# Kernel tuning notes

Hardware: AMD Instinct MI355X
Metric: run time of the kernel (lower is better)

## Reference

```python
import jax, jax.numpy as jnp
import numpy as np

K = 27        # num_neighs
EPS = 1e-5    # BatchNorm eps (torch default)
LATENT = 256


def _knn_idx(pts, k):
    # pts: (B, N, 3) -> (B, N, k) indices of k nearest points (self included, dist 0),
    # matching torch_cluster.knn(x, x, k).
    d = jnp.sum((pts[:, :, None, :] - pts[:, None, :, :]) ** 2, axis=-1)  # (B, N, N)
    _, idx = jax.lax.top_k(-d, k)
    return idx


def _graph_feature(x, idx):
    # x: (B, C, N), idx: (B, N, K) -> (B, 2C, N, K) = concat(neigh - center, center)
    xt = jnp.transpose(x, (0, 2, 1))               # (B, N, C)
    neigh = jax.vmap(lambda p, i: p[i])(xt, idx)   # (B, N, K, C) gather
    center = xt[:, :, None, :]                     # (B, N, 1, C)
    feat = jnp.concatenate([neigh - center, jnp.broadcast_to(center, neigh.shape)], axis=-1)
    return jnp.transpose(feat, (0, 3, 1, 2))       # (B, 2C, N, K)


def _bn_lrelu(x, gamma, beta, axes):
    # Training-mode BatchNorm (biased batch stats over `axes`, channel = dim 1) + LeakyReLU(0.2)
    mean = jnp.mean(x, axis=axes, keepdims=True)
    var = jnp.var(x, axis=axes, keepdims=True)
    shape = [1] * x.ndim
    shape[1] = -1
    y = (x - mean) * jax.lax.rsqrt(var + EPS) * gamma.reshape(shape) + beta.reshape(shape)
    return jnp.where(y >= 0, y, 0.2 * y)


def setup_inputs() -> dict:
    key = jax.random.key(0)
    ks = jax.random.split(key, 6)
    B, T, N = 2, 2, 256
    x = jax.random.normal(ks[0], (B, T, N, 3), dtype=jnp.float32)
    # Conv2d(1x1) channel ladder for depth=4, bb_size=24, input_features=6
    dims = [(6, 48), (192, 192), (768, 768), (3072, 3072)]
    inp = {"x": x}
    for i, (cin, cout) in enumerate(dims):
        inp[f"w{i}"] = jax.random.normal(ks[i + 1], (cout, cin), dtype=jnp.float32) * 0.05
        inp[f"g{i}"] = jnp.ones((cout,), jnp.float32)
        inp[f"b{i}"] = jnp.zeros((cout,), jnp.float32)
    # final Conv1d(8160 -> latent): 8160 = 48*(2+8+32+128)
    inp["w4"] = jax.random.normal(ks[5], (LATENT, 8160), dtype=jnp.float32) * 0.02
    inp["g4"] = jnp.ones((LATENT,), jnp.float32)
    inp["b4"] = jnp.zeros((LATENT,), jnp.float32)
    return inp


def reference(x, w0, g0, b0, w1, g1, b1, w2, g2, b2, w3, g3, b3, w4, g4, b4):
    B, T, N, _ = x.shape
    flat = x.reshape(B * T, N, 3)
    idx = _knn_idx(flat, K)  # fixed neighbors reused at every depth (only_true_neighs=True)
    cur = _graph_feature(jnp.transpose(flat, (0, 2, 1)), idx)  # (BT, 6, N, K)
    outs = []
    for w, g, b in [(w0, g0, b0), (w1, g1, b1), (w2, g2, b2), (w3, g3, b3)]:
        if outs:
            cur = _graph_feature(outs[-1], idx)      # (BT, 2C_prev, N, K)
        h = jnp.einsum('bcnk,oc->bonk', cur, w)      # 1x1 conv, no bias
        h = _bn_lrelu(h, g, b, axes=(0, 2, 3))
        hmax = jnp.max(h, axis=-1)                   # max over K neighbors -> (BT, C, N)
        C = hmax.shape[1]
        exp = hmax.reshape(B, T, C, N)
        # Faithful to source: avgpool does `out, _ = x.mean(dim=1, keepdim=True)` which
        # tuple-unpacks the batch dim (requires B==2): out = batch-0 temporal mean (1, C, N),
        # then expanded to (B, T, C, N).
        tp = jnp.mean(exp, axis=1, keepdims=True)[0]  # (1, C, N)
        comb = jnp.concatenate([exp, jnp.broadcast_to(tp[None], exp.shape)], axis=2)  # (B,T,2C,N)
        outs.append(comb.reshape(B * T, 2 * C, N))
    xcat = jnp.concatenate(outs, axis=1)             # (BT, 8160, N)
    y = jnp.einsum('bcn,oc->bon', xcat, w4)          # 1x1 conv1d
    y = _bn_lrelu(y, g4, b4, axes=(0, 2))
    return y.reshape(B, T, LATENT, N)
```

## Files before the change

kernel.cpp:

```cpp
#include <hip/hip_runtime.h>
#include <hip/hip_bf16.h>

#define NPTS 256
#define NB   4
#define KNN  27
#define EPSV 1e-5f

typedef unsigned short u16;
typedef _Float16 f16;
typedef __attribute__((ext_vector_type(8))) _Float16 f16x8;
typedef __attribute__((ext_vector_type(4))) _Float16 f16x4;
typedef __attribute__((ext_vector_type(4))) float f32x4;

#define OFF_IDX    0
#define OFF_XYZ    131072
#define OFF_A0     262144
#define OFF_A1     270336
#define OFF_A2     344064
#define OFF_A3     1523712
#define OFF_A4     20398080
#define OFF_PQ     24576000
#define OFF_SLICE  74907648
#define OFF_XC     100073472
#define OFF_Y      116785152

typedef __attribute__((address_space(3))) unsigned int lds_u32_t;
typedef __attribute__((address_space(1))) unsigned int glb_u32_t;

__device__ __forceinline__ void gload16(const f16* g, const u16* l) {
    __builtin_amdgcn_global_load_lds((const glb_u32_t*)g, (lds_u32_t*)(u16*)l, 16, 0, 0);
}

__device__ __forceinline__ float dist3_nocontract(float ax, float ay, float az,
                                                  float bx, float by, float bz) {
#pragma clang fp contract(off)
    float dx = bx - ax, dy = by - ay, dz = bz - az;
    float s = dx * dx;
    s = s + dy * dy;
    s = s + dz * dz;
    return s;
}

__global__ __launch_bounds__(256) void knn_prep(
    const float* __restrict__ x, int* __restrict__ idx, f16* __restrict__ xyz,
    const float* __restrict__ w0, const float* __restrict__ w1,
    const float* __restrict__ w2, const float* __restrict__ w3,
    const float* __restrict__ w4, char* __restrict__ ws)
{
    int bid = blockIdx.x;
    int tid = threadIdx.x;

    if (bid < 4096 && (bid & 3) == 3) {
        if (tid >= 64) return;
        int pt = bid >> 2;
        int b = pt >> 8, n = pt & 255;
        int lane = tid;

        float xp0 = x[pt * 3 + 0];
        float xp1 = x[pt * 3 + 1];
        float xp2 = x[pt * 3 + 2];

        if (lane < 32) {
            float v = (lane < 3) ? x[pt * 3 + lane] : 0.f;
            xyz[((long)b * NPTS + n) * 32 + lane] = (f16)v;
        }

        unsigned long long key[4];
#pragma unroll
        for (int u = 0; u < 4; ++u) {
            int j = lane + 64 * u;
            int gj = b * NPTS + j;
            float d = dist3_nocontract(xp0, xp1, xp2,
                                       x[gj * 3 + 0], x[gj * 3 + 1], x[gj * 3 + 2]);
            key[u] = ((unsigned long long)__float_as_uint(d) << 32) | (unsigned int)j;
        }

        for (int r = 0; r < KNN; ++r) {
            unsigned long long m = key[0];
            m = key[1] < m ? key[1] : m;
            m = key[2] < m ? key[2] : m;
            m = key[3] < m ? key[3] : m;
#pragma unroll
            for (int off = 32; off; off >>= 1) {
                unsigned long long o = __shfl_xor(m, off);
                m = o < m ? o : m;
            }
            if (lane == 0) idx[pt * 28 + r] = (int)(m & 0xffffffffu);
#pragma unroll
            for (int u = 0; u < 4; ++u)
                if (key[u] == m) key[u] = ~0ULL;
        }
        return;
    }

    int pbid = (bid < 4096) ? (bid - (bid >> 2)) : (bid - 1024);

    if (pbid == 0) {
        f16* A = (f16*)(ws + OFF_A0);
        int jj = tid >> 2;
        int cc = (tid & 3) * 8;
        if (jj < 48) {
            f16x8 lo = {}, df = {};
#pragma unroll
            for (int j = 0; j < 8; ++j) {
                int c = cc + j;
                if (c < 3) {
                    float a = w0[jj * 6 + c];
                    float b2 = w0[jj * 6 + 3 + c];
                    lo[j] = (f16)a;
                    df[j] = (f16)(b2 - a);
                }
            }
            *(f16x8*)&A[jj * 32 + cc] = lo;
            *(f16x8*)&A[(48 + jj) * 32 + cc] = df;
        }
        if (jj < 32) {
            f16x8 z = {};
            *(f16x8*)&A[(96 + jj) * 32 + cc] = z;
        }
        return;
    }
    if (pbid < 13) {
        f16* A = (f16*)(ws + OFF_A1);
        int j = (pbid - 1) * 16 + (tid >> 4);
        int cc = (tid & 15) * 8;
        if (cc >= 96) return;
        f32x4 a0 = *(const f32x4*)&w1[j * 192 + cc];
        f32x4 a1 = *(const f32x4*)&w1[j * 192 + cc + 4];
        f32x4 b0 = *(const f32x4*)&w1[j * 192 + 96 + cc];
        f32x4 b1 = *(const f32x4*)&w1[j * 192 + 96 + cc + 4];
        f16x8 lo, df;
#pragma unroll
        for (int j2 = 0; j2 < 4; ++j2) {
            lo[j2] = (f16)a0[j2];     lo[4 + j2] = (f16)a1[j2];
            df[j2] = (f16)(b0[j2] - a0[j2]);
            df[4 + j2] = (f16)(b1[j2] - a1[j2]);
        }
        *(f16x8*)&A[j * 96 + cc] = lo;
        *(f16x8*)&A[(192 + j) * 96 + cc] = df;
        return;
    }
    if (pbid < 205) {
        f16* A = (f16*)(ws + OFF_A2);
        int j = (pbid - 13) * 4 + (tid >> 6);
        int cc = (tid & 63) * 8;
        if (cc >= 384) return;
        f32x4 a0 = *(const f32x4*)&w2[(long)j * 768 + cc];
        f32x4 a1 = *(const f32x4*)&w2[(long)j * 768 + cc + 4];
        f32x4 b0 = *(const f32x4*)&w2[(long)j * 768 + 384 + cc];
        f32x4 b1 = *(const f32x4*)&w2[(long)j * 768 + 384 + cc + 4];
        f16x8 lo, df;
#pragma unroll
        for (int j2 = 0; j2 < 4; ++j2) {
            lo[j2] = (f16)a0[j2];     lo[4 + j2] = (f16)a1[j2];
            df[j2] = (f16)(b0[j2] - a0[j2]);
            df[4 + j2] = (f16)(b1[j2] - a1[j2]);
        }
        *(f16x8*)&A[(long)j * 384 + cc] = lo;
        *(f16x8*)&A[(long)(768 + j) * 384 + cc] = df;
        return;
    }
    if (pbid < 3277) {
        f16* A = (f16*)(ws + OFF_A3);
        int j = pbid - 205;
        int cc = tid * 8;
        if (cc >= 1536) return;
        f32x4 a0 = *(const f32x4*)&w3[(long)j * 3072 + cc];
        f32x4 a1 = *(const f32x4*)&w3[(long)j * 3072 + cc + 4];
        f32x4 b0 = *(const f32x4*)&w3[(long)j * 3072 + 1536 + cc];
        f32x4 b1 = *(const f32x4*)&w3[(long)j * 3072 + 1536 + cc + 4];
        f16x8 lo, df;
#pragma unroll
        for (int j2 = 0; j2 < 4; ++j2) {
            lo[j2] = (f16)a0[j2];     lo[4 + j2] = (f16)a1[j2];
            df[j2] = (f16)(b0[j2] - a0[j2]);
            df[4 + j2] = (f16)(b1[j2] - a1[j2]);
        }
        *(f16x8*)&A[(long)j * 1536 + cc] = lo;
        *(f16x8*)&A[(long)(3072 + j) * 1536 + cc] = df;
        return;
    }
    {
        f16* A = (f16*)(ws + OFF_A4);
        int loc = pbid - 3277;
        int r = loc >> 2;
        int c0 = (loc & 3) * 2048 + tid * 8;
        if (c0 >= 8160) return;
        f32x4 a0 = *(const f32x4*)&w4[(long)r * 8160 + c0];
        f32x4 a1 = *(const f32x4*)&w4[(long)r * 8160 + c0 + 4];
        f16x8 hv;
#pragma unroll
        for (int j2 = 0; j2 < 4; ++j2) {
            hv[j2] = (f16)a0[j2];
            hv[4 + j2] = (f16)a1[j2];
        }
        *(f16x8*)&A[(long)r * 8160 + c0] = hv;
        return;
    }
}

__global__ __launch_bounds__(256) void gemm_mfma(
    const f16* __restrict__ A, const f16* __restrict__ B,
    float* __restrict__ out, int M, int Kpad, int K,
    int ldF, long bsF, long bsO, int nsplit, long pstride)
{
    __shared__ u16 sA[2][128 * 32];
    __shared__ u16 sB[2][128 * 32];

    int bz = blockIdx.z;
    int b = bz / nsplit, slice = bz - b * nsplit;
    int kchunk = (((K + nsplit - 1) / nsplit) + 31) & ~31;
    int kstart = slice * kchunk;
    int kend = K < kstart + kchunk ? K : kstart + kchunk;
    int nt = (kend - kstart) >> 5;

    const f16* pB = B + (long)b * bsF;
    float* Ob = out + (long)slice * pstride + (long)b * bsO;

    int m0 = blockIdx.x * 128, n0 = blockIdx.y * 128;
    int tid = threadIdx.x, lane = tid & 63, wid = tid >> 6;
    int wm = (wid >> 1) * 64, wn = (wid & 1) * 64;
    int lrow = lane & 15, quad = lane >> 4;

    int r0 = wid * 16 + (lane >> 2);
    int r1 = 64 + r0;
    int ck = lane & 3;
    int c0 = (ck ^ ((r0 >> 1) & 3)) * 8;
    int c1 = (ck ^ ((r1 >> 1) & 3)) * 8;

    const f16* gA0 = A + (long)(m0 + r0) * Kpad + c0 + kstart;
    const f16* gA1 = A + (long)(m0 + r1) * Kpad + c1 + kstart;
    const f16* gB0 = pB + (long)(n0 + r0) * ldF + c0 + kstart;
    const f16* gB1 = pB + (long)(n0 + r1) * ldF + c1 + kstart;

    int oA0 = (wid * 16) * 32;
    int oA1 = (64 + wid * 16) * 32;

    int fs = (quad ^ ((lrow >> 1) & 3)) * 8;
    int offA = (wm + lrow) * 32 + fs;
    int offB = (wn + lrow) * 32 + fs;

    f32x4 acc[4][4] = {};

    gload16(gA0, &sA[0][oA0]);
    gload16(gA1, &sA[0][oA1]);
    gload16(gB0, &sB[0][oA0]);
    gload16(gB1, &sB[0][oA1]);
    gA0 += 32; gA1 += 32; gB0 += 32; gB1 += 32;
    asm volatile("s_waitcnt vmcnt(0)" ::: "memory");
    __builtin_amdgcn_s_barrier();

    for (int t = 0; t < nt - 1; ++t) {
        int cur = t & 1, nxt = cur ^ 1;
        gload16(gA0, &sA[nxt][oA0]);
        gload16(gA1, &sA[nxt][oA1]);
        gload16(gB0, &sB[nxt][oA0]);
        gload16(gB1, &sB[nxt][oA1]);
        gA0 += 32; gA1 += 32; gB0 += 32; gB1 += 32;

        f16x8 fb[4];
#pragma unroll
        for (int nt4 = 0; nt4 < 4; ++nt4)
            fb[nt4] = *(const f16x8*)&sB[cur][offB + nt4 * 512];
        __builtin_amdgcn_s_setprio(1);
#pragma unroll
        for (int mt = 0; mt < 4; ++mt) {
            f16x8 fa = *(const f16x8*)&sA[cur][offA + mt * 512];
#pragma unroll
            for (int nt4 = 0; nt4 < 4; ++nt4)
                acc[mt][nt4] = __builtin_amdgcn_mfma_f32_16x16x32_f16(fa, fb[nt4], acc[mt][nt4], 0, 0, 0);
        }
        __builtin_amdgcn_s_setprio(0);

        asm volatile("s_waitcnt vmcnt(0) lgkmcnt(0)" ::: "memory");
        __builtin_amdgcn_s_barrier();
    }

    {
        int cur = (nt - 1) & 1;
        f16x8 fb[4];
#pragma unroll
        for (int nt4 = 0; nt4 < 4; ++nt4)
            fb[nt4] = *(const f16x8*)&sB[cur][offB + nt4 * 512];
#pragma unroll
        for (int mt = 0; mt < 4; ++mt) {
            f16x8 fa = *(const f16x8*)&sA[cur][offA + mt * 512];
#pragma unroll
            for (int nt4 = 0; nt4 < 4; ++nt4)
                acc[mt][nt4] = __builtin_amdgcn_mfma_f32_16x16x32_f16(fa, fb[nt4], acc[mt][nt4], 0, 0, 0);
        }
    }

#pragma unroll
    for (int mt = 0; mt < 4; ++mt)
#pragma unroll
        for (int nt4 = 0; nt4 < 4; ++nt4) {
            int C = n0 + wn + nt4 * 16 + lrow;
            int Rb = m0 + wm + mt * 16 + quad * 4;
#pragma unroll
            for (int r = 0; r < 4; ++r) {
                int R = Rb + r;
                if (R < M) Ob[(long)R * NPTS + C] = acc[mt][nt4][r];
            }
        }
}

__global__ __launch_bounds__(512) void gather_finalize(
    const float* __restrict__ PQ, long pstride, int nsplit,
    const int* __restrict__ idx,
    const float* __restrict__ g, const float* __restrict__ beta,
    f16* __restrict__ slice, int Co)
{
    __shared__ float p_sh[NB][NPTS];
    __shared__ float val_sh[NB][NPTS];
    __shared__ float red[2][NB][2];
    int o = blockIdx.x;
    int tid = threadIdx.x;
    int b = tid >> 7;
    int l128 = tid & 127;
    int wh = (tid >> 6) & 1;

    long ip0 = ((long)b * 2 * Co + o) * NPTS;
    long iq0 = ((long)b * 2 * Co + Co + o) * NPTS;

    float qv[2];
#pragma unroll
    for (int u = 0; u < 2; ++u) {
        int n = l128 + 128 * u;
        float v = 0.f, q = 0.f;
        for (int sp2 = 0; sp2 < nsplit; ++sp2) {
            v += PQ[sp2 * pstride + ip0 + n];
            q += PQ[sp2 * pstride + iq0 + n];
        }
        p_sh[b][n] = v;
        qv[u] = q;
    }
    __syncthreads();

    float mx[2], mn[2];
    float s = 0.f, ss = 0.f;
#pragma unroll
    for (int u = 0; u < 2; ++u) {
        int n = l128 + 128 * u;
        const int4* ip4 = (const int4*)(idx + ((long)b * NPTS + n) * 28);
        int nb[28];
#pragma unroll
        for (int w = 0; w < 7; ++w) {
            int4 t = ip4[w];
            nb[4 * w] = t.x; nb[4 * w + 1] = t.y;
            nb[4 * w + 2] = t.z; nb[4 * w + 3] = t.w;
        }
        float sp = 0.f, spp = 0.f;
        float pmx = -__builtin_inff(), pmn = __builtin_inff();
#pragma unroll
        for (int k = 0; k < KNN; ++k) {
            float p = p_sh[b][nb[k]];
            sp += p;
            spp = fmaf(p, p, spp);
            pmx = fmaxf(pmx, p);
            pmn = fminf(pmn, p);
        }
        float q = qv[u];
        s += sp + 27.f * q;
        ss += spp + q * fmaf(2.f, sp, 27.f * q);
        mx[u] = pmx + q;
        mn[u] = pmn + q;
    }
#pragma unroll
    for (int off = 32; off; off >>= 1) {
        s += __shfl_xor(s, off);
        ss += __shfl_xor(ss, off);
    }
    if ((tid & 63) == 0) { red[0][b][wh] = s; red[1][b][wh] = ss; }
    __syncthreads();

    float ts = ((red[0][0][0] + red[0][0][1]) + (red[0][1][0] + red[0][1][1]))
             + ((red[0][2][0] + red[0][2][1]) + (red[0][3][0] + red[0][3][1]));
    float tss = ((red[1][0][0] + red[1][0][1]) + (red[1][1][0] + red[1][1][1]))
              + ((red[1][2][0] + red[1][2][1]) + (red[1][3][0] + red[1][3][1]));
    const float cnt = (float)(NB * NPTS * KNN);
    float mean = ts / cnt;
    float var = tss / cnt - mean * mean;
    float sc = g[o] * (1.0f / sqrtf(var + EPSV));
    float tt = beta[o] - mean * sc;

#pragma unroll
    for (int u = 0; u < 2; ++u) {
        int n = l128 + 128 * u;
        float v = (sc >= 0.f) ? mx[u] : mn[u];
        float z = sc * v + tt;
        val_sh[b][n] = z >= 0.f ? z : 0.2f * z;
    }
    __syncthreads();

    long ro = ((long)b * 2 * Co + o) * NPTS;
    long rt = ((long)b * 2 * Co + Co + o) * NPTS;
#pragma unroll
    for (int u = 0; u < 2; ++u) {
        int n = l128 + 128 * u;
        float tp = 0.5f * (val_sh[0][n] + val_sh[1][n]);
        slice[ro + n] = (f16)val_sh[b][n];
        slice[rt + n] = (f16)tp;
    }
}

__global__ __launch_bounds__(256) void transpose_cn(
    const f16* __restrict__ slice, f16* __restrict__ xc,
    int Ctot, int offc)
{
    __shared__ u16 t[32][36];
    int c0 = blockIdx.x * 32, n0 = blockIdx.y * 32, b = blockIdx.z;
    const f16* S = slice + (long)b * Ctot * NPTS;
    int tid = threadIdx.x;
    int r = tid >> 3, s4 = (tid & 7) * 4;

    f16x4 v = *(const f16x4*)&S[(long)(c0 + r) * NPTS + n0 + s4];
    t[r][s4 + 0] = ((const u16*)&v)[0];
    t[r][s4 + 1] = ((const u16*)&v)[1];
    t[r][s4 + 2] = ((const u16*)&v)[2];
    t[r][s4 + 3] = ((const u16*)&v)[3];
    __syncthreads();

    long base = ((long)b * NPTS + n0 + r) * 8160 + offc + c0 + s4;
    f16x4 hv;
    u16* hp = (u16*)&hv;
#pragma unroll
    for (int j = 0; j < 4; ++j) hp[j] = t[s4 + j][r];
    *(f16x4*)&xc[base] = hv;
}

__global__ __launch_bounds__(256) void final_bn(const float* __restrict__ y,
                                                const float* __restrict__ g4,
                                                const float* __restrict__ b4,
                                                float* __restrict__ out) {
    __shared__ float red[8];
    int o = blockIdx.x;
    int tid = threadIdx.x;
    int lane = tid & 63, w = tid >> 6;

    float v[4];
    float s = 0.f, ss = 0.f;
#pragma unroll
    for (int b = 0; b < 4; ++b) {
        float acc = 0.f;
#pragma unroll
        for (int sp = 0; sp < 16; ++sp)
            acc += y[sp * 262144 + b * 65536 + o * 256 + tid];
        v[b] = acc;
        s += acc;
        ss += acc * acc;
    }
#pragma unroll
    for (int off = 32; off; off >>= 1) {
        s += __shfl_xor(s, off);
        ss += __shfl_xor(ss, off);
    }
    if (lane == 0) { red[w] = s; red[4 + w] = ss; }
    __syncthreads();
    s = (red[0] + red[1]) + (red[2] + red[3]);
    ss = (red[4] + red[5]) + (red[6] + red[7]);
    float mean = s / 1024.f;
    float var = ss / 1024.f - mean * mean;
    float sc = g4[o] * (1.0f / sqrtf(var + EPSV));
    float tt = b4[o] - mean * sc;
#pragma unroll
    for (int b = 0; b < 4; ++b) {
        float z = sc * v[b] + tt;
        z = z >= 0.f ? z : 0.2f * z;
        out[(long)b * 65536 + o * 256 + tid] = z;
    }
}

extern "C" void kernel_launch(void* const* d_in, const int* in_sizes, int n_in,
                              void* d_out, int out_size, void* d_ws, size_t ws_size,
                              hipStream_t stream) {
    const float* x = (const float*)d_in[0];
    const float* wl[4];
    const float* gl[4];
    const float* bl[4];
    for (int i = 0; i < 4; ++i) {
        wl[i] = (const float*)d_in[1 + 3 * i];
        gl[i] = (const float*)d_in[2 + 3 * i];
        bl[i] = (const float*)d_in[3 + 3 * i];
    }
    const float* w4 = (const float*)d_in[13];
    const float* g4 = (const float*)d_in[14];
    const float* b4 = (const float*)d_in[15];

    char* ws = (char*)d_ws;
    int* idx = (int*)(ws + OFF_IDX);
    f16* xyz = (f16*)(ws + OFF_XYZ);
    float* PQ = (float*)(ws + OFF_PQ);
    f16* slice = (f16*)(ws + OFF_SLICE);
    f16* xc = (f16*)(ws + OFF_XC);
    float* y = (float*)(ws + OFF_Y);

    knn_prep<<<dim3(5325), dim3(256), 0, stream>>>(x, idx, xyz,
                                                   wl[0], wl[1], wl[2], wl[3], w4, ws);

    const int Kp[4] = {32, 96, 384, 1536};
    const int Co[4] = {48, 192, 768, 3072};
    const int offc[4] = {0, 96, 480, 2016};
    const int inoff[4] = {0, 0, 96, 480};
    const int nsp[4] = {1, 3, 2, 1};
    const long aoff[4] = {OFF_A0, OFF_A1, OFF_A2, OFF_A3};

    for (int i = 0; i < 4; ++i) {
        int M = 2 * Co[i];
        int Mpad = (M + 127) & ~127;
        const f16* A = (const f16*)(ws + aoff[i]);

        const f16* Bp;
        int ldF;
        long bsF;
        if (i == 0) { Bp = xyz; ldF = 32; bsF = (long)NPTS * 32; }
        else { Bp = xc + inoff[i]; ldF = 8160; bsF = (long)NPTS * 8160; }

        long pstride = (long)NB * M * NPTS;
        gemm_mfma<<<dim3(Mpad / 128, NPTS / 128, NB * nsp[i]), dim3(256), 0, stream>>>(
            A, Bp, PQ, M, Kp[i], Kp[i], ldF, bsF, (long)M * NPTS, nsp[i], pstride);

        gather_finalize<<<dim3(Co[i]), dim3(512), 0, stream>>>(
            PQ, pstride, nsp[i], idx, gl[i], bl[i], slice, Co[i]);
        transpose_cn<<<dim3(M / 32, NPTS / 32, NB), dim3(256), 0, stream>>>(
            slice, xc, M, offc[i]);
    }

    gemm_mfma<<<dim3(2, 2, NB * 16), dim3(256), 0, stream>>>(
        (const f16*)(ws + OFF_A4), xc, y, 256, 8160, 8160, 8160,
        (long)NPTS * 8160, (long)256 * NPTS, 16, (long)NB * 256 * NPTS);
    final_bn<<<dim3(256), dim3(256), 0, stream>>>(y, g4, b4, (float*)d_out);
}
```

Measured before the change: 272.1 us.

## Deepen GEMM shared-memory pipeline to four stages with partial vmcnt waits

Replaces the double-buffered LDS pipeline in the MFMA GEMM with a four-buffer ring that keeps up to three K-tiles of global-to-LDS loads in flight. Uses partial s_waitcnt vmcnt counts instead of draining all loads each iteration, and needs only one barrier per iteration. The goal is to hide global memory latency behind MFMA work. It doubles LDS use per block to 64KB, which may lower occupancy. Whether one barrier is enough to protect buffer reuse depends on the ring distance.

Measured after the change: 255.3 us. 1.07x faster.

```diff
diff --git a/kernel.cpp b/kernel.cpp
--- a/kernel.cpp
+++ b/kernel.cpp
@@ -204,8 +204,7 @@
     float* __restrict__ out, int M, int Kpad, int K,
     int ldF, long bsF, long bsO, int nsplit, long pstride)
 {
-    __shared__ u16 sA[2][128 * 32];
-    __shared__ u16 sB[2][128 * 32];
+    __shared__ u16 sS[4][2][4096];
 
     int bz = blockIdx.z;
     int b = bz / nsplit, slice = bz - b * nsplit;
@@ -242,54 +241,45 @@
 
     f32x4 acc[4][4] = {};
 
-    gload16(gA0, &sA[0][oA0]);
-    gload16(gA1, &sA[0][oA1]);
-    gload16(gB0, &sB[0][oA0]);
-    gload16(gB1, &sB[0][oA1]);
-    gA0 += 32; gA1 += 32; gB0 += 32; gB1 += 32;
-    asm volatile("s_waitcnt vmcnt(0)" ::: "memory");
-    __builtin_amdgcn_s_barrier();
-
-    for (int t = 0; t < nt - 1; ++t) {
-        int cur = t & 1, nxt = cur ^ 1;
-        gload16(gA0, &sA[nxt][oA0]);
-        gload16(gA1, &sA[nxt][oA1]);
-        gload16(gB0, &sB[nxt][oA0]);
-        gload16(gB1, &sB[nxt][oA1]);
-        gA0 += 32; gA1 += 32; gB0 += 32; gB1 += 32;
-
+#define STAGE(bf)                                                  \
+    do {                                                           \
+        gload16(gA0, &sS[bf][0][oA0]);                             \
+        gload16(gA1, &sS[bf][0][oA1]);                             \
+        gload16(gB0, &sS[bf][1][oA0]);                             \
+        gload16(gB1, &sS[bf][1][oA1]);                             \
+        gA0 += 32; gA1 += 32; gB0 += 32; gB1 += 32;                \
+    } while (0)
+
+    STAGE(0);
+    if (nt > 1) STAGE(1);
+    if (nt > 2) STAGE(2);
+
+    for (int t = 0; t < nt; ++t) {
+        int rem = nt - 1 - t;
+        if (rem >= 2)      asm volatile("s_waitcnt vmcnt(8)" ::: "memory");
+        else if (rem == 1) asm volatile("s_waitcnt vmcnt(4)" ::: "memory");
+        else               asm volatile("s_waitcnt vmcnt(0)" ::: "memory");
+        __builtin_amdgcn_s_barrier();
+
+        if (t + 3 < nt) STAGE((t + 3) & 3);
+
+        const u16* bA = &sS[t & 3][0][0];
+        const u16* bB = &sS[t & 3][1][0];
         f16x8 fb[4];
 #pragma unroll
         for (int nt4 = 0; nt4 < 4; ++nt4)
-            fb[nt4] = *(const f16x8*)&sB[cur][offB + nt4 * 512];
+            fb[nt4] = *(const f16x8*)&bB[offB + nt4 * 512];
         __builtin_amdgcn_s_setprio(1);
 #pragma unroll
         for (int mt = 0; mt < 4; ++mt) {
-            f16x8 fa = *(const f16x8*)&sA[cur][offA + mt * 512];
+            f16x8 fa = *(const f16x8*)&bA[offA + mt * 512];
 #pragma unroll
             for (int nt4 = 0; nt4 < 4; ++nt4)
                 acc[mt][nt4] = __builtin_amdgcn_mfma_f32_16x16x32_f16(fa, fb[nt4], acc[mt][nt4], 0, 0, 0);
         }
         __builtin_amdgcn_s_setprio(0);
-
-        asm volatile("s_waitcnt vmcnt(0) lgkmcnt(0)" ::: "memory");
-        __builtin_amdgcn_s_barrier();
-    }
-
-    {
-        int cur = (nt - 1) & 1;
-        f16x8 fb[4];
-#pragma unroll
-        for (int nt4 = 0; nt4 < 4; ++nt4)
-            fb[nt4] = *(const f16x8*)&sB[cur][offB + nt4 * 512];
-#pragma unroll
-        for (int mt = 0; mt < 4; ++mt) {
-            f16x8 fa = *(const f16x8*)&sA[cur][offA + mt * 512];
-#pragma unroll
-            for (int nt4 = 0; nt4 < 4; ++nt4)
-                acc[mt][nt4] = __builtin_amdgcn_mfma_f32_16x16x32_f16(fa, fb[nt4], acc[mt][nt4], 0, 0, 0);
-        }
-    }
+    }
+#undef STAGE
 
 #pragma unroll
     for (int mt = 0; mt < 4; ++mt)
```

## Double GEMM K-tile to 64 with wider swizzle and single-barrier pipeline

Applied to the files above, without the earlier changes.

The MFMA GEMM now stages 64-wide K tiles in LDS instead of 32, using an 8-way XOR swizzle. Each staged tile feeds two MFMA sub-steps, and the second sub-step is skipped for half-filled tail tiles. The double-buffer loop is restructured so there is one wait and barrier per iteration, and the layer-1 split-K factor drops from 3 to 2 to fit the larger chunk. The aim is to halve barrier and loop overhead per FLOP and issue fewer, larger loads. In exchange, LDS use doubles, which can reduce occupancy, and tail tiles read padding past the valid K range.

Result: no change. 269.2 us (-1.1%).

```diff
diff --git a/kernel.cpp b/kernel.cpp
--- a/kernel.cpp
+++ b/kernel.cpp
@@ -204,15 +204,15 @@
     float* __restrict__ out, int M, int Kpad, int K,
     int ldF, long bsF, long bsO, int nsplit, long pstride)
 {
-    __shared__ u16 sA[2][128 * 32];
-    __shared__ u16 sB[2][128 * 32];
+    __shared__ u16 sA[2][128 * 64];
+    __shared__ u16 sB[2][128 * 64];
 
     int bz = blockIdx.z;
     int b = bz / nsplit, slice = bz - b * nsplit;
-    int kchunk = (((K + nsplit - 1) / nsplit) + 31) & ~31;
+    int kchunk = (((K + nsplit - 1) / nsplit) + 63) & ~63;
     int kstart = slice * kchunk;
     int kend = K < kstart + kchunk ? K : kstart + kchunk;
-    int nt = (kend - kstart) >> 5;
+    int nt = (kend - kstart + 63) >> 6;
 
     const f16* pB = B + (long)b * bsF;
     float* Ob = out + (long)slice * pstride + (long)b * bsO;
@@ -222,74 +222,77 @@
     int wm = (wid >> 1) * 64, wn = (wid & 1) * 64;
     int lrow = lane & 15, quad = lane >> 4;
 
-    int r0 = wid * 16 + (lane >> 2);
-    int r1 = 64 + r0;
-    int ck = lane & 3;
-    int c0 = (ck ^ ((r0 >> 1) & 3)) * 8;
-    int c1 = (ck ^ ((r1 >> 1) & 3)) * 8;
-
-    const f16* gA0 = A + (long)(m0 + r0) * Kpad + c0 + kstart;
-    const f16* gA1 = A + (long)(m0 + r1) * Kpad + c1 + kstart;
-    const f16* gB0 = pB + (long)(n0 + r0) * ldF + c0 + kstart;
-    const f16* gB1 = pB + (long)(n0 + r1) * ldF + c1 + kstart;
-
-    int oA0 = (wid * 16) * 32;
-    int oA1 = (64 + wid * 16) * 32;
-
-    int fs = (quad ^ ((lrow >> 1) & 3)) * 8;
-    int offA = (wm + lrow) * 32 + fs;
-    int offB = (wn + lrow) * 32 + fs;
+    int r = tid >> 3;
+    int ck = tid & 7;
+    int scol = (ck ^ (r & 7)) * 8;
+
+    const f16* gA0 = A + (long)(m0 + r) * Kpad + scol + kstart;
+    const f16* gB0 = pB + (long)(n0 + r) * ldF + scol + kstart;
+    long off32A = 32L * Kpad;
+    long off32B = 32L * ldF;
+
+    int fs0 = (quad ^ (lrow & 7)) * 8;
+    int fs1 = ((quad + 4) ^ (lrow & 7)) * 8;
+    int offA = (wm + lrow) * 64;
+    int offB = (wn + lrow) * 64;
 
     f32x4 acc[4][4] = {};
 
-    gload16(gA0, &sA[0][oA0]);
-    gload16(gA1, &sA[0][oA1]);
-    gload16(gB0, &sB[0][oA0]);
-    gload16(gB1, &sB[0][oA1]);
-    gA0 += 32; gA1 += 32; gB0 += 32; gB1 += 32;
-    asm volatile("s_waitcnt vmcnt(0)" ::: "memory");
-    __builtin_amdgcn_s_barrier();
-
-    for (int t = 0; t < nt - 1; ++t) {
-        int cur = t & 1, nxt = cur ^ 1;
-        gload16(gA0, &sA[nxt][oA0]);
-        gload16(gA1, &sA[nxt][oA1]);
-        gload16(gB0, &sB[nxt][oA0]);
-        gload16(gB1, &sB[nxt][oA1]);
-        gA0 += 32; gA1 += 32; gB0 += 32; gB1 += 32;
+#define STAGE(bf)                                                   \
+    do {                                                            \
+        gload16(gA0,              &sA[bf][(0  + wid * 8) * 64]);    \
+        gload16(gA0 + off32A,     &sA[bf][(32 + wid * 8) * 64]);    \
+        gload16(gA0 + 2 * off32A, &sA[bf][(64 + wid * 8) * 64]);    \
+        gload16(gA0 + 3 * off32A, &sA[bf][(96 + wid * 8) * 64]);    \
+        gload16(gB0,              &sB[bf][(0  + wid * 8) * 64]);    \
+        gload16(gB0 + off32B,     &sB[bf][(32 + wid * 8) * 64]);    \
+        gload16(gB0 + 2 * off32B, &sB[bf][(64 + wid * 8) * 64]);    \
+        gload16(gB0 + 3 * off32B, &sB[bf][(96 + wid * 8) * 64]);    \
+        gA0 += 64; gB0 += 64;                                       \
+    } while (0)
+
+    if (nt > 0) STAGE(0);
+
+    for (int t = 0; t < nt; ++t) {
+        asm volatile("s_waitcnt vmcnt(0)" ::: "memory");
+        __builtin_amdgcn_s_barrier();
+
+        if (t + 1 < nt) STAGE((t + 1) & 1);
+
+        const u16* bA = &sA[t & 1][0];
+        const u16* bB = &sB[t & 1][0];
+        int kk = kstart + (t << 6);
 
         f16x8 fb[4];
 #pragma unroll
         for (int nt4 = 0; nt4 < 4; ++nt4)
-            fb[nt4] = *(const f16x8*)&sB[cur][offB + nt4 * 512];
+            fb[nt4] = *(const f16x8*)&bB[offB + nt4 * 1024 + fs0];
         __builtin_amdgcn_s_setprio(1);
 #pragma unroll
         for (int mt = 0; mt < 4; ++mt) {
-            f16x8 fa = *(const f16x8*)&sA[cur][offA + mt * 512];
+            f16x8 fa = *(const f16x8*)&bA[offA + mt * 1024 + fs0];
 #pragma unroll
             for (int nt4 = 0; nt4 < 4; ++nt4)
                 acc[mt][nt4] = __builtin_amdgcn_mfma_f32_16x16x32_f16(fa, fb[nt4], acc[mt][nt4], 0, 0, 0);
         }
         __builtin_amdgcn_s_setprio(0);
 
-        asm volatile("s_waitcnt vmcnt(0) lgkmcnt(0)" ::: "memory");
-        __builtin_amdgcn_s_barrier();
-    }
-
-    {
-        int cur = (nt - 1) & 1;
-        f16x8 fb[4];
-#pragma unroll
-        for (int nt4 = 0; nt4 < 4; ++nt4)
-            fb[nt4] = *(const f16x8*)&sB[cur][offB + nt4 * 512];
-#pragma unroll
-        for (int mt = 0; mt < 4; ++mt) {
-            f16x8 fa = *(const f16x8*)&sA[cur][offA + mt * 512];
+        if (kk + 32 < kend) {
 #pragma unroll
             for (int nt4 = 0; nt4 < 4; ++nt4)
-                acc[mt][nt4] = __builtin_amdgcn_mfma_f32_16x16x32_f16(fa, fb[nt4], acc[mt][nt4], 0, 0, 0);
-        }
-    }
+                fb[nt4] = *(const f16x8*)&bB[offB + nt4 * 1024 + fs1];
+            __builtin_amdgcn_s_setprio(1);
+#pragma unroll
+            for (int mt = 0; mt < 4; ++mt) {
+                f16x8 fa = *(const f16x8*)&bA[offA + mt * 1024 + fs1];
+#pragma unroll
+                for (int nt4 = 0; nt4 < 4; ++nt4)
+                    acc[mt][nt4] = __builtin_amdgcn_mfma_f32_16x16x32_f16(fa, fb[nt4], acc[mt][nt4], 0, 0, 0);
+            }
+            __builtin_amdgcn_s_setprio(0);
+        }
+    }
+#undef STAGE
 
 #pragma unroll
     for (int mt = 0; mt < 4; ++mt)
@@ -298,9 +301,9 @@
             int C = n0 + wn + nt4 * 16 + lrow;
             int Rb = m0 + wm + mt * 16 + quad * 4;
 #pragma unroll
-            for (int r = 0; r < 4; ++r) {
-                int R = Rb + r;
-                if (R < M) Ob[(long)R * NPTS + C] = acc[mt][nt4][r];
+            for (int rr = 0; rr < 4; ++rr) {
+                int R = Rb + rr;
+                if (R < M) Ob[(long)R * NPTS + C] = acc[mt][nt4][rr];
             }
         }
 }
@@ -502,7 +505,7 @@
     const int Co[4] = {48, 192, 768, 3072};
     const int offc[4] = {0, 96, 480, 2016};
     const int inoff[4] = {0, 0, 96, 480};
-    const int nsp[4] = {1, 3, 2, 1};
+    const int nsp[4] = {1, 2, 2, 1};
     const long aoff[4] = {OFF_A0, OFF_A1, OFF_A2, OFF_A3};
 
     for (int i = 0; i < 4; ++i) {
@@ -526,7 +529,7 @@
             slice, xc, M, offc[i]);
     }
 
-    gemm_mfma<<<dim3(2, 2, NB * 16), dim3(256), 0, stream>>>(
+    gemm_mfma<<<dim3(2, NPTS / 128, NB * 16), dim3(256), 0, stream>>>(
         (const f16*)(ws + OFF_A4), xc, y, 256, 8160, 8160, 8160,
         (long)NPTS * 8160, (long)256 * NPTS, 16, (long)NB * 256 * NPTS);
     final_bn<<<dim3(256), dim3(256), 0, stream>>>(y, g4, b4, (float*)d_out);
```
